# Kernel tuning notes

Measured on AMD Instinct MI355X. Metric: run time of the kernel, lower is better.

Reference implementation:

```python
import jax, jax.numpy as jnp
import numpy as np

B = 2000          # graphs in batch
LGPG = 100        # line-graph nodes per graph
NPG = 20          # original nodes per graph
ELPG = 10         # labeled edges per graph
D = 300           # cfg.gnn.dim_inner
HDIM = D // 3
N_LG = B * LGPG
N_NODES = B * NPG
E_LAB = B * ELPG
LGVARIANT = 21


def setup_inputs() -> dict:
    key = jax.random.key(0)
    k1, k2, k3 = jax.random.split(key, 3)
    x = jax.random.normal(k1, (N_LG, D), jnp.float32)
    # local original-node indices per line-graph node
    lg_node_idx = jax.random.randint(k2, (N_LG, 2), 0, NPG, dtype=jnp.int32)
    ptr = jnp.arange(B + 1, dtype=jnp.int32) * LGPG           # line-graph ptr
    org_graph_size = jnp.full((B,), NPG, dtype=jnp.int32)
    edge_label_size = jnp.full((B,), ELPG, dtype=jnp.int32)
    # global line-graph indices, valid within each graph's slice
    local = jax.random.randint(k3, (2, E_LAB), 0, LGPG, dtype=jnp.int32)
    offs = jnp.repeat(jnp.arange(B, dtype=jnp.int32) * LGPG, ELPG)
    edge_index_labeled = local + offs[None, :]
    return {"x": x, "lg_node_idx": lg_node_idx, "ptr": ptr,
            "org_graph_size": org_graph_size, "edge_label_size": edge_label_size,
            "edge_index_labeled": edge_index_labeled}


def _segment_mean(x, seg, num_segments):
    sums = jax.ops.segment_sum(x, seg, num_segments=num_segments)
    cnts = jax.ops.segment_sum(jnp.ones((x.shape[0],), x.dtype), seg,
                               num_segments=num_segments)
    return jnp.where(cnts[:, None] > 0, sums / jnp.maximum(cnts, 1)[:, None], 0.0)


def reference(x, lg_node_idx, ptr, org_graph_size, edge_label_size, edge_index_labeled):
    n_lg = x.shape[0]
    # exclusive cumsum of original graph sizes = per-graph node offset
    node_off = jnp.cumsum(org_graph_size) - org_graph_size            # [B]
    lg_sizes = ptr[1:] - ptr[:-1]                                     # [B]
    padding = jnp.repeat(node_off, lg_sizes, total_repeat_length=n_lg)  # [N_lg]
    padded = lg_node_idx + padding[:, None]                           # [N_lg, 2] global node idx
    outgoing = _segment_mean(x, padded[:, 0], N_NODES)                # [N, D]
    incoming = _segment_mean(x, padded[:, 1], N_NODES)                # [N, D]
    if LGVARIANT in (21, 30):
        x_new = jnp.concatenate([incoming[:, :2 * HDIM], outgoing[:, 2 * HDIM:]], axis=1)
    elif LGVARIANT == 22:
        x_new = jnp.concatenate([(incoming[:, :HDIM] + outgoing[:, :HDIM]) * 0.5,
                                 incoming[:, HDIM:2 * HDIM], outgoing[:, 2 * HDIM:]], axis=1)
    else:
        x_new = incoming - outgoing
    # line-graph offsets (exclusive cumsum of line-graph sizes)
    lg_off = jnp.cumsum(lg_sizes) - lg_sizes                          # [B] == ptr[:-1]-ptr[0]
    e_lab = edge_index_labeled.shape[1]
    lg_padding = jnp.repeat(lg_off, edge_label_size, total_repeat_length=e_lab)
    edge_index_labeled_new = edge_index_labeled - lg_padding[None, :]
    ptr_new = jnp.concatenate([jnp.zeros((1,), org_graph_size.dtype),
                               jnp.cumsum(org_graph_size)])
    batch_vec = jnp.repeat(jnp.arange(org_graph_size.shape[0], dtype=jnp.int32),
                           org_graph_size, total_repeat_length=N_NODES)
    return x_new, edge_index_labeled_new, ptr_new, batch_vec
```

## Files before the change

### kernel.cpp

```cpp
#include <hip/hip_runtime.h>
#include <hip/hip_bf16.h>

#define D_      300
#define G2_     150
#define NPGMAX  20
#define LGPG_   100
#define ELPG_   10
#define BN_     2000
#define NNODES_ 40000
#define ELAB_   20000
#define TPB_    192
#define BATCH_  8
#define POOLSZ  (LGPG_ + 3 * BATCH_)

__global__ __launch_bounds__(TPB_) void main_kernel(
    const float* __restrict__ x, const int* __restrict__ lgidx,
    const int* __restrict__ edge_in,
    float* __restrict__ out)
{
    float* __restrict__ out_x     = out;
    float* __restrict__ out_edge  = out + (size_t)NNODES_ * D_;
    float* __restrict__ out_ptr   = out + (size_t)NNODES_ * D_ + 2 * ELAB_;
    float* __restrict__ out_batch = out + (size_t)NNODES_ * D_ + 2 * ELAB_ + (BN_ + 1);

    __shared__ int   sidx[LGPG_ * 2];
    __shared__ int   pool_in[POOLSZ], pool_out[POOLSZ];
    __shared__ float inv_in[NPGMAX], inv_out[NPGMAX];
    __shared__ int   cnt_in[NPGMAX], cnt_out[NPGMAX];
    __shared__ int   off_in[NPGMAX + 1], off_out[NPGMAX + 1];

    const int g = blockIdx.x;
    const int t = threadIdx.x;

    const int nbase = NPGMAX * g;
    const int eb    = ELPG_ * g;
    const int lg0   = LGPG_ * g;
    const int lgoff = lg0;

    if (t < NPGMAX) { cnt_in[t] = 0; cnt_out[t] = 0; }
    for (int i = t; i < POOLSZ; i += TPB_) { pool_in[i] = 0; pool_out[i] = 0; }
    for (int i = t; i < LGPG_ * 2; i += TPB_) sidx[i] = lgidx[(size_t)lg0 * 2 + i];
    __syncthreads();

    if (t < LGPG_) {
        atomicAdd(&cnt_out[sidx[2 * t]], 1);
        atomicAdd(&cnt_in[sidx[2 * t + 1]], 1);
    }
    __syncthreads();

    if (t == 0) {
        int a = 0, b = 0;
        for (int n = 0; n < NPGMAX; ++n) {
            off_in[n] = a;  a += cnt_in[n];
            off_out[n] = b; b += cnt_out[n];
        }
        off_in[NPGMAX] = a; off_out[NPGMAX] = b;
    }
    __syncthreads();

    if (t < NPGMAX) {
        const int ci = cnt_in[t], co = cnt_out[t];
        inv_in[t]  = (ci > 0) ? 1.0f / (float)ci : 0.0f;
        inv_out[t] = (co > 0) ? 1.0f / (float)co : 0.0f;
    }

    if (t < LGPG_) {
        const int nin = sidx[2 * t + 1], nou = sidx[2 * t];
        int pin = 0, pou = 0;
        for (int r = 0; r < t; ++r) {
            pin += (sidx[2 * r + 1] == nin);
            pou += (sidx[2 * r]     == nou);
        }
        const int si = off_in[nin] + pin;
        const int so = off_out[nou] + pou;
        pool_in[si]  = (t * G2_) | (((si == off_in[nin + 1] - 1) ? (nin + 1) : 0) << 15);
        pool_out[so] = (t * G2_) | (((so == off_out[nou + 1] - 1) ? (nou + 1) : 0) << 15);
    }
    __syncthreads();

    if (t < G2_) {
        const int q = t;
        const bool inc = (q < 100);
        const int*   __restrict__ pool = inc ? pool_in : pool_out;
        const int*   __restrict__ off  = inc ? off_in  : off_out;
        const float* __restrict__ invc = inc ? inv_in  : inv_out;
        const float2* __restrict__ xg2 = (const float2*)(x + (size_t)lg0 * D_) + q;
        float2* __restrict__ outp2 = (float2*)(out_x + (size_t)nbase * D_) + q;

        for (int n = 0; n < NPGMAX; ++n)
            if (off[n + 1] == off[n]) outp2[(size_t)n * G2_] = make_float2(0.0f, 0.0f);

        const int total  = LGPG_;
        const int totalp = (total + 2 * BATCH_ - 1) & ~(2 * BATCH_ - 1);
        float sx = 0.0f, sy = 0.0f;

        int    pa[BATCH_], pb[BATCH_];
        float2 va[BATCH_], vb[BATCH_];

        #pragma unroll
        for (int j = 0; j < BATCH_; ++j) {
            pa[j] = pool[j];
            va[j] = xg2[pa[j] & 0x7FFF];
        }

        for (int k = 0; k < totalp; k += 2 * BATCH_) {
            #pragma unroll
            for (int j = 0; j < BATCH_; ++j) {
                pb[j] = pool[k + BATCH_ + j];
                vb[j] = xg2[pb[j] & 0x7FFF];
            }
            #pragma unroll
            for (int j = 0; j < BATCH_; ++j) {
                const int kk = k + j;
                if (kk < total) {
                    sx += va[j].x; sy += va[j].y;
                    const int e = pa[j] >> 15;
                    if (e) {
                        const float iv = invc[e - 1];
                        outp2[(size_t)(e - 1) * G2_] = make_float2(sx * iv, sy * iv);
                        sx = 0.0f; sy = 0.0f;
                    }
                }
            }
            #pragma unroll
            for (int j = 0; j < BATCH_; ++j) {
                pa[j] = pool[k + 2 * BATCH_ + j];
                va[j] = xg2[pa[j] & 0x7FFF];
            }
            #pragma unroll
            for (int j = 0; j < BATCH_; ++j) {
                const int kk = k + BATCH_ + j;
                if (kk < total) {
                    sx += vb[j].x; sy += vb[j].y;
                    const int e = pb[j] >> 15;
                    if (e) {
                        const float iv = invc[e - 1];
                        outp2[(size_t)(e - 1) * G2_] = make_float2(sx * iv, sy * iv);
                        sx = 0.0f; sy = 0.0f;
                    }
                }
            }
        }
    }

    if (t == 0) {
        out_ptr[g + 1] = (float)(nbase + NPGMAX);
        if (g == 0) out_ptr[0] = 0.0f;
    }
    if (t < NPGMAX)
        out_batch[nbase + t] = (float)g;

    if (t < ELPG_) {
        out_edge[eb + t]                 = (float)(edge_in[eb + t] - lgoff);
        out_edge[(size_t)ELAB_ + eb + t] = (float)(edge_in[(size_t)ELAB_ + eb + t] - lgoff);
    }
}

extern "C" void kernel_launch(void* const* d_in, const int* in_sizes, int n_in,
                              void* d_out, int out_size, void* d_ws, size_t ws_size,
                              hipStream_t stream)
{
    const float* x        = (const float*)d_in[0];
    const int*   lgidx    = (const int*)d_in[1];
    const int*   edge_in  = (const int*)d_in[5];

    main_kernel<<<BN_, TPB_, 0, stream>>>(x, lgidx, edge_in, (float*)d_out);
}
```

Baseline: 58.35 us.

## Process two graphs per block with 320 threads and fully unroll gather loop

Each block now handles two graphs: it uses 320 threads split into two halves of 160, duplicates the shared-memory structures per graph, and launches half as many blocks. The main gather loop gets a fixed trip count so it can be fully unrolled. The aim is to amortize per-block setup and barrier latency and to cut the serial prefix-sum and other single-thread phases per graph. In exchange, each block uses more shared memory and registers, and there are fewer blocks to spread across the CUs.

```diff
diff --git a/kernel.cpp b/kernel.cpp
--- a/kernel.cpp
+++ b/kernel.cpp
@@ -3,13 +3,14 @@
 
 #define D_      300
 #define G2_     150
-#define NPGMAX  20
+#define NPG_    20
 #define LGPG_   100
 #define ELPG_   10
 #define BN_     2000
 #define NNODES_ 40000
 #define ELAB_   20000
-#define TPB_    192
+#define HALF_   160
+#define TPB_    320
 #define BATCH_  8
 #define POOLSZ  (LGPG_ + 3 * BATCH_)
 
@@ -23,77 +24,78 @@
     float* __restrict__ out_ptr   = out + (size_t)NNODES_ * D_ + 2 * ELAB_;
     float* __restrict__ out_batch = out + (size_t)NNODES_ * D_ + 2 * ELAB_ + (BN_ + 1);
 
-    __shared__ int   sidx[LGPG_ * 2];
-    __shared__ int   pool_in[POOLSZ], pool_out[POOLSZ];
-    __shared__ float inv_in[NPGMAX], inv_out[NPGMAX];
-    __shared__ int   cnt_in[NPGMAX], cnt_out[NPGMAX];
-    __shared__ int   off_in[NPGMAX + 1], off_out[NPGMAX + 1];
+    __shared__ int   sidx[2][LGPG_ * 2];
+    __shared__ int   pool_in[2][POOLSZ], pool_out[2][POOLSZ];
+    __shared__ float inv_in[2][NPG_], inv_out[2][NPG_];
+    __shared__ int   cnt_in[2][NPG_], cnt_out[2][NPG_];
+    __shared__ int   off_in[2][NPG_ + 1], off_out[2][NPG_ + 1];
 
-    const int g = blockIdx.x;
+    const int gbase = 2 * blockIdx.x;
     const int t = threadIdx.x;
 
-    const int nbase = NPGMAX * g;
-    const int eb    = ELPG_ * g;
-    const int lg0   = LGPG_ * g;
-    const int lgoff = lg0;
-
-    if (t < NPGMAX) { cnt_in[t] = 0; cnt_out[t] = 0; }
-    for (int i = t; i < POOLSZ; i += TPB_) { pool_in[i] = 0; pool_out[i] = 0; }
-    for (int i = t; i < LGPG_ * 2; i += TPB_) sidx[i] = lgidx[(size_t)lg0 * 2 + i];
-    __syncthreads();
-
-    if (t < LGPG_) {
-        atomicAdd(&cnt_out[sidx[2 * t]], 1);
-        atomicAdd(&cnt_in[sidx[2 * t + 1]], 1);
+    for (int i = t; i < 2 * NPG_; i += TPB_) { cnt_in[i / NPG_][i % NPG_] = 0; cnt_out[i / NPG_][i % NPG_] = 0; }
+    for (int i = t; i < 2 * POOLSZ; i += TPB_) { pool_in[i / POOLSZ][i % POOLSZ] = 0; pool_out[i / POOLSZ][i % POOLSZ] = 0; }
+    for (int i = t; i < 2 * LGPG_ * 2; i += TPB_) {
+        const int gi = i / (LGPG_ * 2), j = i - gi * (LGPG_ * 2);
+        sidx[gi][j] = lgidx[(size_t)(LGPG_ * (gbase + gi)) * 2 + j];
     }
     __syncthreads();
 
-    if (t == 0) {
-        int a = 0, b = 0;
-        for (int n = 0; n < NPGMAX; ++n) {
-            off_in[n] = a;  a += cnt_in[n];
-            off_out[n] = b; b += cnt_out[n];
-        }
-        off_in[NPGMAX] = a; off_out[NPGMAX] = b;
+    if (t < 2 * LGPG_) {
+        const int gi = t / LGPG_, r = t - gi * LGPG_;
+        atomicAdd(&cnt_out[gi][sidx[gi][2 * r]], 1);
+        atomicAdd(&cnt_in[gi][sidx[gi][2 * r + 1]], 1);
     }
     __syncthreads();
 
-    if (t < NPGMAX) {
-        const int ci = cnt_in[t], co = cnt_out[t];
-        inv_in[t]  = (ci > 0) ? 1.0f / (float)ci : 0.0f;
-        inv_out[t] = (co > 0) ? 1.0f / (float)co : 0.0f;
-    }
-
-    if (t < LGPG_) {
-        const int nin = sidx[2 * t + 1], nou = sidx[2 * t];
-        int pin = 0, pou = 0;
-        for (int r = 0; r < t; ++r) {
-            pin += (sidx[2 * r + 1] == nin);
-            pou += (sidx[2 * r]     == nou);
+    if (t < 2) {
+        int a = 0, b = 0;
+        for (int n = 0; n < NPG_; ++n) {
+            off_in[t][n] = a;  a += cnt_in[t][n];
+            off_out[t][n] = b; b += cnt_out[t][n];
         }
-        const int si = off_in[nin] + pin;
-        const int so = off_out[nou] + pou;
-        pool_in[si]  = (t * G2_) | (((si == off_in[nin + 1] - 1) ? (nin + 1) : 0) << 15);
-        pool_out[so] = (t * G2_) | (((so == off_out[nou + 1] - 1) ? (nou + 1) : 0) << 15);
+        off_in[t][NPG_] = a; off_out[t][NPG_] = b;
     }
     __syncthreads();
 
-    if (t < G2_) {
-        const int q = t;
-        const bool inc = (q < 100);
-        const int*   __restrict__ pool = inc ? pool_in : pool_out;
-        const int*   __restrict__ off  = inc ? off_in  : off_out;
-        const float* __restrict__ invc = inc ? inv_in  : inv_out;
-        const float2* __restrict__ xg2 = (const float2*)(x + (size_t)lg0 * D_) + q;
-        float2* __restrict__ outp2 = (float2*)(out_x + (size_t)nbase * D_) + q;
+    if (t < 2 * NPG_) {
+        const int gi = t / NPG_, n = t - gi * NPG_;
+        const int ci = cnt_in[gi][n], co = cnt_out[gi][n];
+        inv_in[gi][n]  = (ci > 0) ? 1.0f / (float)ci : 0.0f;
+        inv_out[gi][n] = (co > 0) ? 1.0f / (float)co : 0.0f;
+    }
 
-        for (int n = 0; n < NPGMAX; ++n)
+    if (t < 2 * LGPG_) {
+        const int gi = t / LGPG_, r = t - gi * LGPG_;
+        const int nin = sidx[gi][2 * r + 1], nou = sidx[gi][2 * r];
+        int pin = 0, pou = 0;
+        for (int rr = 0; rr < r; ++rr) {
+            pin += (sidx[gi][2 * rr + 1] == nin);
+            pou += (sidx[gi][2 * rr]     == nou);
+        }
+        const int si = off_in[gi][nin] + pin;
+        const int so = off_out[gi][nou] + pou;
+        pool_in[gi][si]  = (r * G2_) | (((si == off_in[gi][nin + 1] - 1) ? (nin + 1) : 0) << 15);
+        pool_out[gi][so] = (r * G2_) | (((so == off_out[gi][nou + 1] - 1) ? (nou + 1) : 0) << 15);
+    }
+    __syncthreads();
+
+    const int gi = t / HALF_;
+    const int q  = t - gi * HALF_;
+    if (q < G2_) {
+        const bool inc = (q < LGPG_);
+        const int*   __restrict__ pool = inc ? pool_in[gi] : pool_out[gi];
+        const int*   __restrict__ off  = inc ? off_in[gi]  : off_out[gi];
+        const float* __restrict__ invc = inc ? inv_in[gi]  : inv_out[gi];
+        const float2* __restrict__ xg2 =
+            (const float2*)(x + (size_t)(LGPG_ * (gbase + gi)) * D_) + q;
+        float2* __restrict__ outp2 =
+            (float2*)(out_x + (size_t)(NPG_ * (gbase + gi)) * D_) + q;
+
+        for (int n = 0; n < NPG_; ++n)
             if (off[n + 1] == off[n]) outp2[(size_t)n * G2_] = make_float2(0.0f, 0.0f);
 
-        const int total  = LGPG_;
-        const int totalp = (total + 2 * BATCH_ - 1) & ~(2 * BATCH_ - 1);
         float sx = 0.0f, sy = 0.0f;
-
         int    pa[BATCH_], pb[BATCH_];
         float2 va[BATCH_], vb[BATCH_];
 
@@ -103,7 +105,8 @@
             va[j] = xg2[pa[j] & 0x7FFF];
         }
 
-        for (int k = 0; k < totalp; k += 2 * BATCH_) {
+        #pragma unroll
+        for (int k = 0; k < 112; k += 2 * BATCH_) {
             #pragma unroll
             for (int j = 0; j < BATCH_; ++j) {
                 pb[j] = pool[k + BATCH_ + j];
@@ -111,8 +114,7 @@
             }
             #pragma unroll
             for (int j = 0; j < BATCH_; ++j) {
-                const int kk = k + j;
-                if (kk < total) {
+                if (k + j < LGPG_) {
                     sx += va[j].x; sy += va[j].y;
                     const int e = pa[j] >> 15;
                     if (e) {
@@ -129,8 +131,7 @@
             }
             #pragma unroll
             for (int j = 0; j < BATCH_; ++j) {
-                const int kk = k + BATCH_ + j;
-                if (kk < total) {
+                if (k + BATCH_ + j < LGPG_) {
                     sx += vb[j].x; sy += vb[j].y;
                     const int e = pb[j] >> 15;
                     if (e) {
@@ -143,16 +144,19 @@
         }
     }
 
-    if (t == 0) {
-        out_ptr[g + 1] = (float)(nbase + NPGMAX);
-        if (g == 0) out_ptr[0] = 0.0f;
-    }
-    if (t < NPGMAX)
-        out_batch[nbase + t] = (float)g;
-
-    if (t < ELPG_) {
-        out_edge[eb + t]                 = (float)(edge_in[eb + t] - lgoff);
-        out_edge[(size_t)ELAB_ + eb + t] = (float)(edge_in[(size_t)ELAB_ + eb + t] - lgoff);
+    {
+        const int g = gbase + gi;
+        const int nbase = NPG_ * g, eb = ELPG_ * g, lg0v = LGPG_ * g;
+        if (q == 0) {
+            out_ptr[g + 1] = (float)(nbase + NPG_);
+            if (g == 0) out_ptr[0] = 0.0f;
+        }
+        if (q < NPG_)
+            out_batch[nbase + q] = (float)g;
+        if (q < ELPG_) {
+            out_edge[eb + q]                 = (float)(edge_in[eb + q] - lg0v);
+            out_edge[(size_t)ELAB_ + eb + q] = (float)(edge_in[(size_t)ELAB_ + eb + q] - lg0v);
+        }
     }
 }
 
@@ -164,5 +168,5 @@
     const int*   lgidx    = (const int*)d_in[1];
     const int*   edge_in  = (const int*)d_in[5];
 
-    main_kernel<<<BN_, TPB_, 0, stream>>>(x, lgidx, edge_in, (float*)d_out);
+    main_kernel<<<BN_ / 2, TPB_, 0, stream>>>(x, lgidx, edge_in, (float*)d_out);
 }
```

After: 60.01 us. +2.8%, slower.
